# Kernel tuning notes

Measured on AMD Instinct MI355X. Metric: run time of the kernel, lower is better.

## Reference

```python
import jax, jax.numpy as jnp
import numpy as np

B, S, HID, H = 8, 1024, 2048, 16
D = HID // H  # head dim 128
MAX_LEN, SCALE_BASE, THETA_BASE, EPS = 1024, 512.0, 10000.0, 1e-5


def setup_inputs() -> dict:
    key = jax.random.key(0)
    ks = jax.random.split(key, 10)
    std = 0.02
    n_layers_scale = std / np.sqrt(24.0)
    return {
        "activations": jax.random.normal(ks[0], (B, S, HID), jnp.float32),
        "cache_k": jnp.zeros((B, MAX_LEN, H, D), jnp.float32),
        "cache_v": jnp.zeros((B, MAX_LEN, H, D), jnp.float32),
        "index": 0,
        "ln1_w": jnp.ones((HID,), jnp.float32),
        "ln2_w": jnp.ones((HID,), jnp.float32),
        "q_w": std * jax.random.normal(ks[1], (HID, HID), jnp.float32),
        "k_w": std * jax.random.normal(ks[2], (HID, HID), jnp.float32),
        "v_w": std * jax.random.normal(ks[3], (HID, HID), jnp.float32),
        "o_w": n_layers_scale * jax.random.normal(ks[4], (HID, HID), jnp.float32),
        "w1": std * jax.random.normal(ks[5], (4 * HID, HID), jnp.float32),
        "w2": n_layers_scale * jax.random.normal(ks[6], (HID, 4 * HID), jnp.float32),
    }


def _ln(x, w):
    m = jnp.mean(x, axis=-1, keepdims=True)
    v = jnp.mean((x - m) ** 2, axis=-1, keepdims=True)
    return (x - m) * jax.lax.rsqrt(v + EPS) * w


def _rotate_every_two(x):
    return jnp.stack((-x[..., 1::2], x[..., 0::2]), axis=-1).reshape(x.shape)


def _xpos_consts(start, end):
    drange = jnp.arange(2, D + 2, 2, dtype=jnp.float32)
    theta = jnp.repeat((1.0 / THETA_BASE) ** (drange / D), 2)
    alpha = 0.4 * D
    zeta = jnp.repeat((drange / (D / 2) + alpha) / (1 + alpha), 2)
    half = MAX_LEN // 2
    seq = (jnp.arange(-half, MAX_LEN - half, dtype=jnp.float32) / SCALE_BASE)[start:end]
    seq = seq[:, None, None]  # [S,1,1]
    c = jnp.cos(seq * theta[None, None, :])  # [S,1,D]
    s = jnp.sin(seq * theta[None, None, :])
    t = zeta[None, None, :] ** seq
    return c, s, t


def reference(activations, cache_k, cache_v, index, ln1_w, ln2_w, q_w, k_w, v_w, o_w, w1, w2):
    xn = _ln(activations, ln1_w)
    q = (xn @ q_w.T).reshape(B, S, H, D)
    k = (xn @ k_w.T).reshape(B, S, H, D)
    v = (xn @ v_w.T).reshape(B, S, H, D)
    # NOTE: source applies xpos to (keys, values), exactly as written
    c, s, t = _xpos_consts(index, index + S)
    k = (k * c + _rotate_every_two(k) * s) * t
    v = (v * c + _rotate_every_two(v) * s) / t
    # index==0 and S==MAX_LEN -> get_full_kv returns incoming kv, mask None (causal)
    scale = 1.0 / np.sqrt(D)
    scores = jnp.einsum("bqhd,bkhd->bhqk", q, k) * scale
    causal = jnp.tril(jnp.ones((S, S), bool))
    scores = jnp.where(causal[None, None], scores, -jnp.inf)
    attn = jax.nn.softmax(scores, axis=-1)
    ctx = jnp.einsum("bhqk,bkhd->bqhd", attn, v).reshape(B, S, HID)
    acts = activations + ctx @ o_w.T
    h = jax.nn.gelu(_ln(acts, ln2_w) @ w1.T, approximate=False)
    acts = acts + h @ w2.T
    return acts, cache_k, cache_v
```

## Files before the change

kernel.cpp:

```cpp
#include <hip/hip_runtime.h>
#include <hip/hip_bf16.h>
#include <math.h>

#define B_ 8
#define S_ 1024
#define HID_ 2048
#define H_ 16
#define D_ 128

typedef __attribute__((ext_vector_type(8))) short bf16x8;
typedef __attribute__((ext_vector_type(4))) float f32x4;

__device__ inline unsigned short f2b_raw(float f){
  union { __hip_bfloat16 h; unsigned short u; } cv; cv.h = __float2bfloat16(f); return cv.u;
}

__device__ inline void async_copy16(const void* g, void* l){
  __builtin_amdgcn_global_load_lds((const __attribute__((address_space(1))) unsigned int*)g,
                                   (__attribute__((address_space(3))) unsigned int*)l, 16, 0, 0);
}

__global__ __launch_bounds__(256) void cvt_all(const float* __restrict__ qw, const float* __restrict__ kw,
                                               const float* __restrict__ vw, const float* __restrict__ ow,
                                               const float* __restrict__ w1, const float* __restrict__ w2,
                                               unsigned short* __restrict__ dst){
  int i = blockIdx.x*256 + threadIdx.x;
  if (i >= 12582912) return;
  const float* src;
  int local;
  if      (i <  1048576){ src = qw; local = i; }
  else if (i <  2097152){ src = kw; local = i - 1048576; }
  else if (i <  3145728){ src = vw; local = i - 2097152; }
  else if (i <  4194304){ src = ow; local = i - 3145728; }
  else if (i <  8388608){ src = w1; local = i - 4194304; }
  else                  { src = w2; local = i - 8388608; }
  float4 f = ((const float4*)src)[local];
  ushort4 o;
  o.x = f2b_raw(f.x); o.y = f2b_raw(f.y); o.z = f2b_raw(f.z); o.w = f2b_raw(f.w);
  ((ushort4*)dst)[i] = o;
}

__global__ __launch_bounds__(256) void ln_kernel(const float* __restrict__ x,
                                                 const float* __restrict__ w,
                                                 unsigned short* __restrict__ y){
  const int row = blockIdx.x, tid = threadIdx.x;
  const float* xr = x + (size_t)row*HID_;
  float4 a = ((const float4*)xr)[tid];
  float4 b = ((const float4*)xr)[tid+256];
  float s  = a.x+a.y+a.z+a.w + b.x+b.y+b.z+b.w;
  float ss = a.x*a.x+a.y*a.y+a.z*a.z+a.w*a.w + b.x*b.x+b.y*b.y+b.z*b.z+b.w*b.w;
  #pragma unroll
  for (int off=1; off<64; off<<=1){ s += __shfl_xor(s, off, 64); ss += __shfl_xor(ss, off, 64); }
  __shared__ float red[8];
  int wv = tid>>6;
  if ((tid&63)==0){ red[wv]=s; red[4+wv]=ss; }
  __syncthreads();
  s  = red[0]+red[1]+red[2]+red[3];
  ss = red[4]+red[5]+red[6]+red[7];
  float mean = s * (1.0f/HID_);
  float var  = ss * (1.0f/HID_) - mean*mean;
  float rstd = rsqrtf(var + 1e-5f);
  float4 w0 = ((const float4*)w)[tid];
  float4 w1v = ((const float4*)w)[tid+256];
  ushort4 o0, o1;
  o0.x = f2b_raw((a.x-mean)*rstd*w0.x); o0.y = f2b_raw((a.y-mean)*rstd*w0.y);
  o0.z = f2b_raw((a.z-mean)*rstd*w0.z); o0.w = f2b_raw((a.w-mean)*rstd*w0.w);
  o1.x = f2b_raw((b.x-mean)*rstd*w1v.x); o1.y = f2b_raw((b.y-mean)*rstd*w1v.y);
  o1.z = f2b_raw((b.z-mean)*rstd*w1v.z); o1.w = f2b_raw((b.w-mean)*rstd*w1v.w);
  *(ushort4*)(y + (size_t)row*HID_ + tid*4) = o0;
  *(ushort4*)(y + (size_t)row*HID_ + 1024 + tid*4) = o1;
}

template<int EPI, int TAG>
__global__ __launch_bounds__(512, 2) void gemm_bt(
    const unsigned short* __restrict__ A, const unsigned short* __restrict__ W,
    unsigned short* __restrict__ out_b, float* __restrict__ out_f,
    const float* __restrict__ res,
    unsigned short* __restrict__ k_out, unsigned short* __restrict__ vt_out,
    const int* __restrict__ idxp,
    int M, int N, int K, float scale)
{
  (void)M;
  __shared__ __align__(16) unsigned short smem[65536];
  const int tid = threadIdx.x;
  const int lane = tid & 63, wv = tid >> 6;
  const int wm = wv >> 2, wn = wv & 3;
  const int lm = lane & 15, lg = lane >> 4;

  const int gx = gridDim.x;
  const int nwg = gx * gridDim.y;
  const int orig = blockIdx.y * gx + blockIdx.x;
  const int wg = (orig & 7) * (nwg >> 3) + (orig >> 3);
  const int bx = wg % gx, by = wg / gx;
  const int m0 = by << 8, n0 = bx << 8;

  f32x4 acc[8][4];
  #pragma unroll
  for (int r=0;r<8;r++)
    #pragma unroll
    for (int c=0;c<4;c++) acc[r][c] = (f32x4){0.f,0.f,0.f,0.f};

  int oA[2], oB[2];
  #pragma unroll
  for (int kc=0;kc<2;kc++){
    const int swz = ((kc*4+lg) ^ (lm&7)) * 8;
    oA[kc] = wm*8192 + lm*64 + swz;
    oB[kc] = wn*4096 + lm*64 + swz;
  }

  int sOffA[2][2], sLdsA[2][2], sOffB[2][2], sLdsB[2][2];
  #pragma unroll
  for (int j=0;j<2;j++){
    const int unit = j*512 + tid;
    const int r7 = unit >> 3, u = unit & 7;
    const int r7g = (unit & ~63) >> 3;
    #pragma unroll
    for (int ch=0; ch<2; ch++){
      const int rowA  = (r7  & 63) + ((r7  & 64) << 1) + ch*64;
      const int rowA0 = (r7g & 63) + ((r7g & 64) << 1) + ch*64;
      sOffA[ch][j] = rowA*K + (u ^ (rowA & 7))*8;
      sLdsA[ch][j] = __builtin_amdgcn_readfirstlane(rowA0*64);
      const int rowB  = (r7  & 31) + ((r7  & 96) << 1) + ch*32;
      const int rowB0 = (r7g & 31) + ((r7g & 96) << 1) + ch*32;
      sOffB[ch][j] = rowB*K + (u ^ (rowB & 7))*8;
      sLdsB[ch][j] = __builtin_amdgcn_readfirstlane(rowB0*64);
    }
  }

  const unsigned short* Ab = A + (size_t)m0 * K;
  const unsigned short* Wb = W + (size_t)n0 * K;

  #pragma unroll
  for (int j=0;j<2;j++){
    async_copy16(Ab + sOffA[0][j], smem + sLdsA[0][j]);
    async_copy16(Ab + sOffA[1][j], smem + sLdsA[1][j]);
    async_copy16(Wb + sOffB[0][j], smem + 16384 + sLdsB[0][j]);
    async_copy16(Wb + sOffB[1][j], smem + 16384 + sLdsB[1][j]);
  }
  asm volatile("s_waitcnt vmcnt(0)\n\ts_barrier" ::: "memory");

  const int T = K >> 6;
  bf16x8 a[4][2], b[4][2];

  for (int t=0; t<T; ++t){
    const int cs = (t & 1) << 15;
    const unsigned short* sAc = smem + cs;
    const unsigned short* sBc = sAc + 16384;
    unsigned short* dA = smem + (cs ^ 32768);
    unsigned short* dB = dA + 16384;
    const int kk = (t + 1) << 6;
    const bool pf = (t + 1 < T);

    #pragma unroll
    for (int r=0;r<4;r++)
      #pragma unroll
      for (int kc=0;kc<2;kc++)
        a[r][kc] = *(const bf16x8*)(sAc + oA[kc] + r*1024);
    #pragma unroll
    for (int c=0;c<2;c++)
      #pragma unroll
      for (int kc=0;kc<2;kc++)
        b[c][kc] = *(const bf16x8*)(sBc + oB[kc] + c*1024);
    if (pf){ async_copy16(Ab + sOffA[0][0] + kk, dA + sLdsA[0][0]);
             async_copy16(Ab + sOffA[0][1] + kk, dA + sLdsA[0][1]);
             async_copy16(Wb + sOffB[0][0] + kk, dB + sLdsB[0][0]);
             async_copy16(Wb + sOffB[0][1] + kk, dB + sLdsB[0][1]);
             async_copy16(Wb + sOffB[1][0] + kk, dB + sLdsB[1][0]);
             async_copy16(Wb + sOffB[1][1] + kk, dB + sLdsB[1][1]);
             async_copy16(Ab + sOffA[1][0] + kk, dA + sLdsA[1][0]);
             async_copy16(Ab + sOffA[1][1] + kk, dA + sLdsA[1][1]);
             asm volatile("s_waitcnt vmcnt(10)\n\ts_barrier" ::: "memory"); }
    else   { asm volatile("s_waitcnt vmcnt(0)\n\ts_barrier" ::: "memory"); }
    __builtin_amdgcn_sched_barrier(0);
    __builtin_amdgcn_s_setprio(1);
    #pragma unroll
    for (int r=0;r<4;r++)
      #pragma unroll
      for (int c=0;c<2;c++)
        #pragma unroll
        for (int kc=0;kc<2;kc++)
          acc[r][c] = __builtin_amdgcn_mfma_f32_16x16x32_bf16(a[r][kc], b[c][kc], acc[r][c], 0,0,0);
    __builtin_amdgcn_s_setprio(0);
    asm volatile("s_barrier" ::: "memory");

    #pragma unroll
    for (int c=0;c<2;c++)
      #pragma unroll
      for (int kc=0;kc<2;kc++)
        b[2+c][kc] = *(const bf16x8*)(sBc + oB[kc] + (2+c)*1024);
    if (pf){ asm volatile("s_waitcnt vmcnt(8)\n\ts_barrier" ::: "memory"); }
    else   { asm volatile("s_barrier" ::: "memory"); }
    __builtin_amdgcn_sched_barrier(0);
    __builtin_amdgcn_s_setprio(1);
    #pragma unroll
    for (int r=0;r<4;r++)
      #pragma unroll
      for (int c=0;c<2;c++)
        #pragma unroll
        for (int kc=0;kc<2;kc++)
          acc[r][2+c] = __builtin_amdgcn_mfma_f32_16x16x32_bf16(a[r][kc], b[2+c][kc], acc[r][2+c], 0,0,0);
    __builtin_amdgcn_s_setprio(0);
    asm volatile("s_barrier" ::: "memory");

    #pragma unroll
    for (int r=0;r<4;r++)
      #pragma unroll
      for (int kc=0;kc<2;kc++)
        a[r][kc] = *(const bf16x8*)(sAc + oA[kc] + 4096 + r*1024);
    asm volatile("s_barrier" ::: "memory");
    __builtin_amdgcn_sched_barrier(0);
    __builtin_amdgcn_s_setprio(1);
    #pragma unroll
    for (int r=0;r<4;r++)
      #pragma unroll
      for (int c=0;c<2;c++)
        #pragma unroll
        for (int kc=0;kc<2;kc++)
          acc[4+r][2+c] = __builtin_amdgcn_mfma_f32_16x16x32_bf16(a[r][kc], b[2+c][kc], acc[4+r][2+c], 0,0,0);
    __builtin_amdgcn_s_setprio(0);
    asm volatile("s_barrier" ::: "memory");

    if (pf){ asm volatile("s_waitcnt vmcnt(4)\n\ts_barrier" ::: "memory"); }
    else   { asm volatile("s_barrier" ::: "memory"); }
    __builtin_amdgcn_sched_barrier(0);
    __builtin_amdgcn_s_setprio(1);
    #pragma unroll
    for (int r=0;r<4;r++)
      #pragma unroll
      for (int c=0;c<2;c++)
        #pragma unroll
        for (int kc=0;kc<2;kc++)
          acc[4+r][c] = __builtin_amdgcn_mfma_f32_16x16x32_bf16(a[r][kc], b[c][kc], acc[4+r][c], 0,0,0);
    __builtin_amdgcn_s_setprio(0);
    asm volatile("s_barrier" ::: "memory");
  }

  if (EPI == 0){
    const int region = n0 >> 11;
    const int idx0 = idxp[0];
    const int b  = m0 >> 10;
    const int s0g = m0 & 1023;
    const int hh = ((n0 & 2047) >> 7) + (wn >> 1);
    const int db = (wn & 1) * 64;
    #pragma unroll
    for (int r=0;r<8;r++){
      #pragma unroll
      for (int c=0;c<4;c++){
        const int srow = s0g + wm*128 + r*16 + lg*4;
        const int d = db + c*16 + lm;
        if (region == 0){
          #pragma unroll
          for (int g=0; g<4; g++)
            out_b[(((size_t)b*H_ + hh)*S_ + srow + g)*D_ + d] = f2b_raw(acc[r][c][g]*scale);
        } else {
          const float fp = (float)((d>>1) + 1);
          const float theta = exp2f(fp * -0.2076205059304601f);
          const float zeta  = (fp*0.03125f + 51.2f) * (1.0f/52.2f);
          const float lz = log2f(zeta);
          const float sgn = (d & 1) ? 1.0f : -1.0f;
          #pragma unroll
          for (int g=0; g<4; g++){
            float va = acc[r][c][g];
            float part = __shfl_xor(va, 1, 64);
            float seq = ((float)(idx0 + srow + g) - 512.0f) * (1.0f/512.0f);
            float ang = seq * theta;
            float sn, cc;
            __sincosf(ang, &sn, &cc);
            float rot = va*cc + sgn*part*sn;
            if (region == 1){
              float tt = exp2f(seq * lz);
              k_out[(((size_t)b*H_ + hh)*S_ + srow + g)*D_ + d] = f2b_raw(rot * tt);
            } else {
              float ti = exp2f(-seq * lz);
              int d_local = wn*64 + c*16 + lm;
              int s_local = wm*128 + r*16 + lg*4 + g;
              int s8 = s_local >> 3;
              smem[d_local*256 + ((s8 ^ (d_local & 7))*8) + (s_local & 7)] = f2b_raw(rot * ti);
            }
          }
        }
      }
    }
    if (region == 2){
      __syncthreads();
      #pragma unroll
      for (int i=0;i<16;i++){
        int f = i*512 + tid;
        int dl = f >> 5, u = f & 31;
        int us = u ^ (dl & 7);
        uint4 val = *(const uint4*)(smem + dl*256 + us*8);
        int hh2 = ((n0 & 2047) >> 7) + (dl >> 7);
        *(uint4*)(vt_out + ((size_t)((size_t)b*H_ + hh2)*D_ + (dl & 127))*S_ + s0g + u*8) = val;
      }
    }
  } else {
    #pragma unroll
    for (int r=0;r<8;r++){
      #pragma unroll
      for (int c=0;c<4;c++){
        const int row0 = m0 + wm*128 + r*16 + lg*4;
        const int col  = n0 + wn*64 + c*16 + lm;
        #pragma unroll
        for (int g=0; g<4; g++){
          float vacc = acc[r][c][g];
          size_t o = (size_t)(row0 + g)*N + col;
          if (EPI == 1){
            out_f[o] = vacc + res[o];
          } else {
            out_b[o] = f2b_raw(0.5f*vacc*(1.0f + erff(vacc*0.70710678118654752f)));
          }
        }
      }
    }
  }
}

__global__ __launch_bounds__(256) void flash_attn(
    const unsigned short* __restrict__ Q, const unsigned short* __restrict__ Kx,
    const unsigned short* __restrict__ VT, unsigned short* __restrict__ ctx)
{
  __shared__ unsigned short sK[64*136];
  __shared__ unsigned short sVT[128*72];
  __shared__ unsigned short sP[4][16*72];
  const int tid = threadIdx.x, lane = tid & 63, wv = tid >> 6;
  const int lm = lane & 15, lg = lane >> 4;
  const int qt = blockIdx.x, bh = blockIdx.y;
  const size_t base = (size_t)bh * S_ * D_;
  const int qr = qt*64 + wv*16;

  bf16x8 aq[4];
  #pragma unroll
  for (int kc=0;kc<4;kc++)
    aq[kc] = *(const bf16x8*)(Q + base + (size_t)(qr + lm)*D_ + kc*32 + lg*8);

  f32x4 accO[8];
  #pragma unroll
  for (int n=0;n<8;n++) accO[n] = (f32x4){0.f,0.f,0.f,0.f};
  float mrow[4] = {-INFINITY,-INFINITY,-INFINITY,-INFINITY};
  float lrow[4] = {0.f,0.f,0.f,0.f};
  unsigned short* myP = &sP[wv][0];

  for (int kt=0; kt<=qt; ++kt){
    int k0 = kt*64;
    __syncthreads();
    #pragma unroll
    for (int i=0;i<4;i++){
      int chunk = i*256 + tid;
      int krow = chunk >> 4, c8 = chunk & 15;
      *(uint4*)(sK + krow*136 + c8*8) = *(const uint4*)(Kx + base + (size_t)(k0+krow)*D_ + c8*8);
      int dd = chunk >> 3, c4 = chunk & 7;
      *(uint4*)(sVT + dd*72 + c4*8) = *(const uint4*)(VT + base + (size_t)dd*S_ + k0 + c4*8);
    }
    __syncthreads();
    f32x4 sc[4];
    #pragma unroll
    for (int n=0;n<4;n++){
      sc[n] = (f32x4){0.f,0.f,0.f,0.f};
      #pragma unroll
      for (int kc=0;kc<4;kc++){
        bf16x8 bk = *(const bf16x8*)(sK + (n*16+lm)*136 + kc*32 + lg*8);
        sc[n] = __builtin_amdgcn_mfma_f32_16x16x32_bf16(aq[kc], bk, sc[n], 0,0,0);
      }
    }
    if (kt == qt){
      #pragma unroll
      for (int n=0;n<4;n++)
        #pragma unroll
        for (int g=0; g<4; g++)
          if (k0 + n*16 + lm > qr + lg*4 + g) sc[n][g] = -INFINITY;
    }
    float mnew[4], alpha[4];
    #pragma unroll
    for (int g=0; g<4; g++){
      float mx = fmaxf(fmaxf(sc[0][g], sc[1][g]), fmaxf(sc[2][g], sc[3][g]));
      #pragma unroll
      for (int off=1; off<16; off<<=1) mx = fmaxf(mx, __shfl_xor(mx, off, 16));
      mnew[g] = fmaxf(mrow[g], mx);
      alpha[g] = __expf(mrow[g] - mnew[g]);
      mrow[g] = mnew[g];
    }
    #pragma unroll
    for (int n=0;n<4;n++)
      #pragma unroll
      for (int g=0; g<4; g++)
        sc[n][g] = __expf(sc[n][g] - mnew[g]);
    #pragma unroll
    for (int g=0; g<4; g++){
      float sum = sc[0][g]+sc[1][g]+sc[2][g]+sc[3][g];
      #pragma unroll
      for (int off=1; off<16; off<<=1) sum += __shfl_xor(sum, off, 16);
      lrow[g] = lrow[g]*alpha[g] + sum;
    }
    #pragma unroll
    for (int n=0;n<8;n++)
      #pragma unroll
      for (int g=0; g<4; g++) accO[n][g] *= alpha[g];
    #pragma unroll
    for (int n=0;n<4;n++)
      #pragma unroll
      for (int g=0; g<4; g++)
        myP[(lg*4+g)*72 + n*16 + lm] = f2b_raw(sc[n][g]);
    #pragma unroll
    for (int kc=0;kc<2;kc++){
      bf16x8 ap = *(const bf16x8*)(myP + lm*72 + kc*32 + lg*8);
      #pragma unroll
      for (int n=0;n<8;n++){
        bf16x8 bv = *(const bf16x8*)(sVT + (n*16+lm)*72 + kc*32 + lg*8);
        accO[n] = __builtin_amdgcn_mfma_f32_16x16x32_bf16(ap, bv, accO[n], 0,0,0);
      }
    }
  }
  const int b = bh >> 4, hh = bh & 15;
  float rl[4];
  #pragma unroll
  for (int g=0; g<4; g++) rl[g] = 1.0f / lrow[g];
  #pragma unroll
  for (int n=0;n<8;n++)
    #pragma unroll
    for (int g=0; g<4; g++){
      int srow = qr + lg*4 + g;
      int d = n*16 + lm;
      ctx[(((size_t)b*S_ + srow)*H_ + hh)*D_ + d] = f2b_raw(accO[n][g]*rl[g]);
    }
}

extern "C" void kernel_launch(void* const* d_in, const int* in_sizes, int n_in,
                              void* d_out, int out_size, void* d_ws, size_t ws_size,
                              hipStream_t stream)
{
  (void)in_sizes; (void)n_in; (void)out_size; (void)ws_size;
  const float* acts   = (const float*)d_in[0];
  const float* cachek = (const float*)d_in[1];
  const float* cachev = (const float*)d_in[2];
  const int*   idxp   = (const int*)d_in[3];
  const float* ln1w   = (const float*)d_in[4];
  const float* ln2w   = (const float*)d_in[5];
  const float* qw     = (const float*)d_in[6];
  const float* kw     = (const float*)d_in[7];
  const float* vw     = (const float*)d_in[8];
  const float* ow     = (const float*)d_in[9];
  const float* w1     = (const float*)d_in[10];
  const float* w2     = (const float*)d_in[11];
  float* out = (float*)d_out;

  unsigned short* wqkv = (unsigned short*)d_ws;
  unsigned short* wo_b = wqkv + 12582912;
  unsigned short* w1_b = wo_b + 4194304;
  unsigned short* w2_b = w1_b + 16777216;
  unsigned short* xn   = w2_b + 16777216;
  unsigned short* qws  = xn   + 16777216;
  unsigned short* kws  = qws  + 16777216;
  unsigned short* vtws = kws  + 16777216;
  unsigned short* ctx  = vtws + 16777216;
  unsigned short* hbuf = qws;

  cvt_all<<<49152, 256, 0, stream>>>(qw, kw, vw, ow, w1, w2, wqkv);

  ln_kernel<<<8192, 256, 0, stream>>>(acts, ln1w, xn);

  gemm_bt<0,0><<<dim3(24,32), 512, 0, stream>>>(xn, wqkv, qws, nullptr, nullptr,
                                                kws, vtws, idxp,
                                                8192, 6144, 2048, 0.08838834764831845f);

  flash_attn<<<dim3(16,128), 256, 0, stream>>>(qws, kws, vtws, ctx);

  gemm_bt<1,1><<<dim3(8,32), 512, 0, stream>>>(ctx, wo_b, nullptr, out, acts,
                                               nullptr, nullptr, nullptr,
                                               8192, 2048, 2048, 1.0f);

  ln_kernel<<<8192, 256, 0, stream>>>(out, ln2w, xn);

  gemm_bt<2,2><<<dim3(32,32), 512, 0, stream>>>(xn, w1_b, hbuf, nullptr, nullptr,
                                                nullptr, nullptr, nullptr,
                                                8192, 8192, 2048, 1.0f);

  gemm_bt<1,3><<<dim3(8,32), 512, 0, stream>>>(hbuf, w2_b, nullptr, out, out,
                                               nullptr, nullptr, nullptr,
                                               8192, 2048, 8192, 1.0f);

  hipMemcpyAsync(out + 16777216, cachek, 67108864ull, hipMemcpyDeviceToDevice, stream);
  hipMemcpyAsync(out + 33554432, cachev, 67108864ull, hipMemcpyDeviceToDevice, stream);
}
```

Before: 1.653 ms.

## Restructure GEMM main loop into two-tile unrolled pipeline with staggered per-chunk prefetch

Unrolls the bf16 GEMM k-loop by two tiles and replaces the single bulk prefetch per tile with per-quadrant async global-to-LDS copies. Each copy is issued right after the LDS region it overwrites has been consumed, so loads for the next tiles overlap the MFMA phases more finely. Waits now use a fixed vmcnt(6) and some barriers are removed. The intent is to hide global load latency and cut barrier stalls. The cost is more complex buffer-reuse ordering and a risk of LDS read/write races if the chunk timing is wrong.

```diff
diff --git a/kernel.cpp b/kernel.cpp
--- a/kernel.cpp
+++ b/kernel.cpp
@@ -71,6 +71,11 @@
   *(ushort4*)(y + (size_t)row*HID_ + 1024 + tid*4) = o1;
 }
 
+#define STAGE_A(ch, kk, dst) { async_copy16(Ab + sOffA[ch][0] + (kk), (dst) + sLdsA[ch][0]); \
+                               async_copy16(Ab + sOffA[ch][1] + (kk), (dst) + sLdsA[ch][1]); }
+#define STAGE_B(ch, kk, dst) { async_copy16(Wb + sOffB[ch][0] + (kk), (dst) + sLdsB[ch][0]); \
+                               async_copy16(Wb + sOffB[ch][1] + (kk), (dst) + sLdsB[ch][1]); }
+
 template<int EPI, int TAG>
 __global__ __launch_bounds__(512, 2) void gemm_bt(
     const unsigned short* __restrict__ A, const unsigned short* __restrict__ W,
@@ -129,48 +134,117 @@
 
   const unsigned short* Ab = A + (size_t)m0 * K;
   const unsigned short* Wb = W + (size_t)n0 * K;
-
-  #pragma unroll
-  for (int j=0;j<2;j++){
-    async_copy16(Ab + sOffA[0][j], smem + sLdsA[0][j]);
-    async_copy16(Ab + sOffA[1][j], smem + sLdsA[1][j]);
-    async_copy16(Wb + sOffB[0][j], smem + 16384 + sLdsB[0][j]);
-    async_copy16(Wb + sOffB[1][j], smem + 16384 + sLdsB[1][j]);
-  }
-  asm volatile("s_waitcnt vmcnt(0)\n\ts_barrier" ::: "memory");
-
-  const int T = K >> 6;
+  const unsigned short* sA0 = smem;
+  const unsigned short* sB0 = smem + 16384;
+  const unsigned short* sA1 = smem + 32768;
+  const unsigned short* sB1 = smem + 49152;
+  unsigned short* dA0 = smem;
+  unsigned short* dB0 = smem + 16384;
+  unsigned short* dA1 = smem + 32768;
+  unsigned short* dB1 = smem + 49152;
+
+  STAGE_A(0, 0, dA0);
+  STAGE_B(0, 0, dB0);
+  STAGE_B(1, 0, dB0);
+  STAGE_A(1, 0, dA0);
+  STAGE_A(0, 64, dA1);
+  STAGE_B(0, 64, dB1);
+  STAGE_B(1, 64, dB1);
+
+  const int T2 = K >> 7;
   bf16x8 a[4][2], b[4][2];
 
-  for (int t=0; t<T; ++t){
-    const int cs = (t & 1) << 15;
-    const unsigned short* sAc = smem + cs;
-    const unsigned short* sBc = sAc + 16384;
-    unsigned short* dA = smem + (cs ^ 32768);
-    unsigned short* dB = dA + 16384;
-    const int kk = (t + 1) << 6;
-    const bool pf = (t + 1 < T);
-
-    #pragma unroll
-    for (int r=0;r<4;r++)
-      #pragma unroll
-      for (int kc=0;kc<2;kc++)
-        a[r][kc] = *(const bf16x8*)(sAc + oA[kc] + r*1024);
+  for (int it=0; it<T2; ++it){
+    const int o1 = (2*it+1) << 6;
+    const int e2 = (2*it+2) << 6;
+    const int o2 = (2*it+3) << 6;
+    const bool pf = (it+1 < T2);
+
+    asm volatile("s_waitcnt vmcnt(6)\n\ts_barrier" ::: "memory");
+    #pragma unroll
+    for (int r=0;r<4;r++)
+      #pragma unroll
+      for (int kc=0;kc<2;kc++)
+        a[r][kc] = *(const bf16x8*)(sA0 + oA[kc] + r*1024);
     #pragma unroll
     for (int c=0;c<2;c++)
       #pragma unroll
       for (int kc=0;kc<2;kc++)
-        b[c][kc] = *(const bf16x8*)(sBc + oB[kc] + c*1024);
-    if (pf){ async_copy16(Ab + sOffA[0][0] + kk, dA + sLdsA[0][0]);
-             async_copy16(Ab + sOffA[0][1] + kk, dA + sLdsA[0][1]);
-             async_copy16(Wb + sOffB[0][0] + kk, dB + sLdsB[0][0]);
-             async_copy16(Wb + sOffB[0][1] + kk, dB + sLdsB[0][1]);
-             async_copy16(Wb + sOffB[1][0] + kk, dB + sLdsB[1][0]);
-             async_copy16(Wb + sOffB[1][1] + kk, dB + sLdsB[1][1]);
-             async_copy16(Ab + sOffA[1][0] + kk, dA + sLdsA[1][0]);
-             async_copy16(Ab + sOffA[1][1] + kk, dA + sLdsA[1][1]);
-             asm volatile("s_waitcnt vmcnt(10)\n\ts_barrier" ::: "memory"); }
+        b[c][kc] = *(const bf16x8*)(sB0 + oB[kc] + c*1024);
+    STAGE_A(1, o1, dA1);
+    __builtin_amdgcn_sched_barrier(0);
+    __builtin_amdgcn_s_setprio(1);
+    #pragma unroll
+    for (int r=0;r<4;r++)
+      #pragma unroll
+      for (int c=0;c<2;c++)
+        #pragma unroll
+        for (int kc=0;kc<2;kc++)
+          acc[r][c] = __builtin_amdgcn_mfma_f32_16x16x32_bf16(a[r][kc], b[c][kc], acc[r][c], 0,0,0);
+    __builtin_amdgcn_s_setprio(0);
+
+    asm volatile("s_barrier" ::: "memory");
+    #pragma unroll
+    for (int c=0;c<2;c++)
+      #pragma unroll
+      for (int kc=0;kc<2;kc++)
+        b[2+c][kc] = *(const bf16x8*)(sB0 + oB[kc] + (2+c)*1024);
+    if (pf) STAGE_A(0, e2, dA0);
+    __builtin_amdgcn_sched_barrier(0);
+    __builtin_amdgcn_s_setprio(1);
+    #pragma unroll
+    for (int r=0;r<4;r++)
+      #pragma unroll
+      for (int c=0;c<2;c++)
+        #pragma unroll
+        for (int kc=0;kc<2;kc++)
+          acc[r][2+c] = __builtin_amdgcn_mfma_f32_16x16x32_bf16(a[r][kc], b[2+c][kc], acc[r][2+c], 0,0,0);
+    __builtin_amdgcn_s_setprio(0);
+
+    asm volatile("s_barrier" ::: "memory");
+    #pragma unroll
+    for (int r=0;r<4;r++)
+      #pragma unroll
+      for (int kc=0;kc<2;kc++)
+        a[r][kc] = *(const bf16x8*)(sA0 + oA[kc] + 4096 + r*1024);
+    if (pf) STAGE_B(0, e2, dB0);
+    __builtin_amdgcn_sched_barrier(0);
+    __builtin_amdgcn_s_setprio(1);
+    #pragma unroll
+    for (int r=0;r<4;r++)
+      #pragma unroll
+      for (int c=0;c<2;c++)
+        #pragma unroll
+        for (int kc=0;kc<2;kc++)
+          acc[4+r][2+c] = __builtin_amdgcn_mfma_f32_16x16x32_bf16(a[r][kc], b[2+c][kc], acc[4+r][2+c], 0,0,0);
+    __builtin_amdgcn_s_setprio(0);
+
+    asm volatile("s_barrier" ::: "memory");
+    if (pf) STAGE_B(1, e2, dB0);
+    __builtin_amdgcn_sched_barrier(0);
+    __builtin_amdgcn_s_setprio(1);
+    #pragma unroll
+    for (int r=0;r<4;r++)
+      #pragma unroll
+      for (int c=0;c<2;c++)
+        #pragma unroll
+        for (int kc=0;kc<2;kc++)
+          acc[4+r][c] = __builtin_amdgcn_mfma_f32_16x16x32_bf16(a[r][kc], b[c][kc], acc[4+r][c], 0,0,0);
+    __builtin_amdgcn_s_setprio(0);
+
+    if (pf){ asm volatile("s_waitcnt vmcnt(6)\n\ts_barrier" ::: "memory"); }
     else   { asm volatile("s_waitcnt vmcnt(0)\n\ts_barrier" ::: "memory"); }
+    #pragma unroll
+    for (int r=0;r<4;r++)
+      #pragma unroll
+      for (int kc=0;kc<2;kc++)
+        a[r][kc] = *(const bf16x8*)(sA1 + oA[kc] + r*1024);
+    #pragma unroll
+    for (int c=0;c<2;c++)
+      #pragma unroll
+      for (int kc=0;kc<2;kc++)
+        b[c][kc] = *(const bf16x8*)(sB1 + oB[kc] + c*1024);
+    if (pf) STAGE_A(1, e2, dA0);
     __builtin_amdgcn_sched_barrier(0);
     __builtin_amdgcn_s_setprio(1);
     #pragma unroll
@@ -181,15 +255,14 @@
         for (int kc=0;kc<2;kc++)
           acc[r][c] = __builtin_amdgcn_mfma_f32_16x16x32_bf16(a[r][kc], b[c][kc], acc[r][c], 0,0,0);
     __builtin_amdgcn_s_setprio(0);
+
     asm volatile("s_barrier" ::: "memory");
-
     #pragma unroll
     for (int c=0;c<2;c++)
       #pragma unroll
       for (int kc=0;kc<2;kc++)
-        b[2+c][kc] = *(const bf16x8*)(sBc + oB[kc] + (2+c)*1024);
-    if (pf){ asm volatile("s_waitcnt vmcnt(8)\n\ts_barrier" ::: "memory"); }
-    else   { asm volatile("s_barrier" ::: "memory"); }
+        b[2+c][kc] = *(const bf16x8*)(sB1 + oB[kc] + (2+c)*1024);
+    if (pf) STAGE_A(0, o2, dA1);
     __builtin_amdgcn_sched_barrier(0);
     __builtin_amdgcn_s_setprio(1);
     #pragma unroll
@@ -200,28 +273,27 @@
         for (int kc=0;kc<2;kc++)
           acc[r][2+c] = __builtin_amdgcn_mfma_f32_16x16x32_bf16(a[r][kc], b[2+c][kc], acc[r][2+c], 0,0,0);
     __builtin_amdgcn_s_setprio(0);
+
     asm volatile("s_barrier" ::: "memory");
-
-    #pragma unroll
-    for (int r=0;r<4;r++)
-      #pragma unroll
-      for (int kc=0;kc<2;kc++)
-        a[r][kc] = *(const bf16x8*)(sAc + oA[kc] + 4096 + r*1024);
+    #pragma unroll
+    for (int r=0;r<4;r++)
+      #pragma unroll
+      for (int kc=0;kc<2;kc++)
+        a[r][kc] = *(const bf16x8*)(sA1 + oA[kc] + 4096 + r*1024);
+    if (pf) STAGE_B(0, o2, dB1);
+    __builtin_amdgcn_sched_barrier(0);
+    __builtin_amdgcn_s_setprio(1);
+    #pragma unroll
+    for (int r=0;r<4;r++)
+      #pragma unroll
+      for (int c=0;c<2;c++)
+        #pragma unroll
+        for (int kc=0;kc<2;kc++)
+          acc[4+r][2+c] = __builtin_amdgcn_mfma_f32_16x16x32_bf16(a[r][kc], b[2+c][kc], acc[4+r][2+c], 0,0,0);
+    __builtin_amdgcn_s_setprio(0);
+
     asm volatile("s_barrier" ::: "memory");
-    __builtin_amdgcn_sched_barrier(0);
-    __builtin_amdgcn_s_setprio(1);
-    #pragma unroll
-    for (int r=0;r<4;r++)
-      #pragma unroll
-      for (int c=0;c<2;c++)
-        #pragma unroll
-        for (int kc=0;kc<2;kc++)
-          acc[4+r][2+c] = __builtin_amdgcn_mfma_f32_16x16x32_bf16(a[r][kc], b[2+c][kc], acc[4+r][2+c], 0,0,0);
-    __builtin_amdgcn_s_setprio(0);
-    asm volatile("s_barrier" ::: "memory");
-
-    if (pf){ asm volatile("s_waitcnt vmcnt(4)\n\ts_barrier" ::: "memory"); }
-    else   { asm volatile("s_barrier" ::: "memory"); }
+    if (pf) STAGE_B(1, o2, dB1);
     __builtin_amdgcn_sched_barrier(0);
     __builtin_amdgcn_s_setprio(1);
     #pragma unroll
@@ -232,7 +304,6 @@
         for (int kc=0;kc<2;kc++)
           acc[4+r][c] = __builtin_amdgcn_mfma_f32_16x16x32_bf16(a[r][kc], b[c][kc], acc[4+r][c], 0,0,0);
     __builtin_amdgcn_s_setprio(0);
-    asm volatile("s_barrier" ::: "memory");
   }
 
   if (EPI == 0){
```

Result: faster. 1.578 ms (-4.5%).
